# Performance work log

Measured on AMD Instinct MI355X. Metric: run time of the kernel, lower is better.

Reference implementation:

```python
import jax, jax.numpy as jnp
import numpy as np

NUM_NODES = 10000
NUM_EDGES = 640000
IN_CH = 128
HID = 128
OUT_CH = 1


def setup_inputs() -> dict:
    key = jax.random.key(0)
    ks = jax.random.split(key, 12)
    x = jax.random.normal(ks[0], (NUM_NODES, IN_CH), dtype=jnp.float32)
    edge_index = jax.random.randint(ks[1], (2, NUM_EDGES), 0, NUM_NODES, dtype=jnp.int64)
    edge_weight = jax.random.uniform(ks[2], (NUM_EDGES,), dtype=jnp.float32)
    s1 = 1.0 / np.sqrt(IN_CH)
    s2 = 1.0 / np.sqrt(HID)
    W1 = jax.random.uniform(ks[3], (HID, IN_CH), minval=-s1, maxval=s1, dtype=jnp.float32)
    b1 = jnp.zeros((HID,), dtype=jnp.float32)
    W2 = jax.random.uniform(ks[4], (HID, HID), minval=-s2, maxval=s2, dtype=jnp.float32)
    b2 = jnp.zeros((HID,), dtype=jnp.float32)
    sc = 1.0 / np.sqrt(HID * 3)
    conv_w = jax.random.uniform(ks[5], (HID, HID, 3), minval=-sc, maxval=sc, dtype=jnp.float32)
    conv_b = jax.random.uniform(ks[6], (HID,), minval=-sc, maxval=sc, dtype=jnp.float32)
    fc_w = jax.random.uniform(ks[7], (OUT_CH, HID), minval=-s2, maxval=s2, dtype=jnp.float32)
    fc_b = jax.random.uniform(ks[8], (OUT_CH,), minval=-s2, maxval=s2, dtype=jnp.float32)
    return {"x": x, "edge_index": edge_index, "edge_weight": edge_weight,
            "W1": W1, "b1": b1, "W2": W2, "b2": b2,
            "conv_w": conv_w, "conv_b": conv_b, "fc_w": fc_w, "fc_b": fc_b}


def _gcn_conv(x, row, col, norm, W, b):
    # PyG GCNConv: linear (no bias in lin), normalized scatter-add, then bias
    xw = x @ W.T                                   # [N, out]
    msg = xw[row] * norm[:, None]                  # gather + edge scale [E, out]
    out = jax.ops.segment_sum(msg, col, num_segments=NUM_NODES)
    return out + b


def reference(x, edge_index, edge_weight, W1, b1, W2, b2, conv_w, conv_b, fc_w, fc_b):
    # gcn_norm with self-loops (fill_value=1.0)
    loop = jnp.arange(NUM_NODES, dtype=edge_index.dtype)
    row = jnp.concatenate([edge_index[0], loop])
    col = jnp.concatenate([edge_index[1], loop])
    w = jnp.concatenate([edge_weight, jnp.ones((NUM_NODES,), dtype=edge_weight.dtype)])
    deg = jax.ops.segment_sum(w, col, num_segments=NUM_NODES)
    dinv = jnp.where(deg > 0, jax.lax.rsqrt(deg), 0.0)
    norm = dinv[row] * w * dinv[col]

    h = jax.nn.relu(_gcn_conv(x, row, col, norm, W1, b1))
    # dropout is identity in eval mode
    h = jax.nn.relu(_gcn_conv(h, row, col, norm, W2, b2))

    # temporal conv1d over node axis: [N,H] -> [1,H,N]
    hc = h.T[None, :, :]
    hc = jax.lax.conv_general_dilated(hc, conv_w, window_strides=(1,),
                                      padding='SAME',
                                      dimension_numbers=('NCH', 'OIH', 'NCH'))
    hc = hc + conv_b[None, :, None]
    h = hc[0].T                                    # [N, H]

    return (h @ fc_w.T + fc_b).squeeze()           # [N]
```

## Files before the change

### kernel.cpp

```cpp
#include <hip/hip_runtime.h>
#include <hip/hip_bf16.h>

#define N_NODES 10000
#define N_EDGES 640000
#define CH 128
#define NB 64
#define EPB (N_EDGES / NB)
#define NCHUNK 40
#define NPAD 10240

__global__ __launch_bounds__(256) void fused_hist_gemm(const int* __restrict__ ei,
        const float* __restrict__ x, const float* __restrict__ W1,
        int* __restrict__ hist, int* __restrict__ pcs, float* __restrict__ out,
        const float* __restrict__ conv_w, const float* __restrict__ conv_b,
        const float* __restrict__ fc_w, const float* __restrict__ fc_b,
        float* __restrict__ vbuf, float* __restrict__ c0) {
    __shared__ __align__(16) char smem[NPAD * 4];
    int t = threadIdx.x;
    int bid = blockIdx.x;
    if (bid < NB) {
        int* h = (int*)smem;
        for (int i = t; i < NPAD; i += 256) h[i] = 0;
        __syncthreads();
        int e0 = bid * EPB;
        for (int i = t; i < EPB; i += 256)
            atomicAdd(&h[ei[N_EDGES + e0 + i]], 1);
        __syncthreads();
        for (int i = t; i < N_NODES; i += 256)
            hist[bid * N_NODES + i] = h[i];
        int lane = t & 63, wave = t >> 6;
        for (int cch = wave; cch < NCHUNK; cch += 4) {
            int s = h[cch * 256 + lane] + h[cch * 256 + lane + 64]
                  + h[cch * 256 + lane + 128] + h[cch * 256 + lane + 192];
            #pragma unroll
            for (int off = 32; off > 0; off >>= 1) s += __shfl_down(s, off, 64);
            if (lane == 0) pcs[cch * NB + bid] = s;
        }
        return;
    }
    if (bid == NB + (N_NODES + 63) / 64) {
        for (int i = t; i <= 384; i += 256) {
            if (i < 384) {
                float s = 0.0f;
                for (int o = 0; o < CH; ++o) s += fc_w[o] * conv_w[o * 384 + i];
                vbuf[i] = s;
            } else {
                float s = fc_b[0];
                for (int o = 0; o < CH; ++o) s += fc_w[o] * conv_b[o];
                *c0 = s;
            }
        }
        return;
    }
    float (*As)[68]  = (float(*)[68])smem;
    float (*Ws)[132] = (float(*)[132])(smem + 32 * 68 * sizeof(float));
    int tx = t & 31;
    int ty = t >> 5;
    int row0 = (bid - NB) * 64;
    float acc[8][4] = {};
    for (int k0 = 0; k0 < 128; k0 += 32) {
        #pragma unroll
        for (int i = 0; i < 8; ++i) {
            int idx = t + i * 256;
            int r = idx >> 5, k = idx & 31;
            int gr = row0 + r;
            As[k][r] = (gr < N_NODES) ? x[gr * CH + k0 + k] : 0.0f;
        }
        #pragma unroll
        for (int i = 0; i < 16; ++i) {
            int idx = t + i * 256;
            int o = idx >> 5, k = idx & 31;
            Ws[k][o] = W1[o * CH + k0 + k];
        }
        __syncthreads();
        #pragma unroll
        for (int kk = 0; kk < 32; ++kk) {
            float a[8], w[4];
            #pragma unroll
            for (int j = 0; j < 8; ++j) a[j] = As[kk][ty * 8 + j];
            #pragma unroll
            for (int c = 0; c < 4; ++c) w[c] = Ws[kk][tx * 4 + c];
            #pragma unroll
            for (int j = 0; j < 8; ++j)
                #pragma unroll
                for (int c = 0; c < 4; ++c)
                    acc[j][c] += a[j] * w[c];
        }
        __syncthreads();
    }
    #pragma unroll
    for (int j = 0; j < 8; ++j) {
        int gr = row0 + ty * 8 + j;
        if (gr < N_NODES) {
            float4 v = make_float4(acc[j][0], acc[j][1], acc[j][2], acc[j][3]);
            *reinterpret_cast<float4*>(&out[gr * CH + tx * 4]) = v;
        }
    }
}

__global__ __launch_bounds__(256) void bofs_kernel(int* __restrict__ hist,
        const int* __restrict__ pcs, int* __restrict__ tot,
        int* __restrict__ offs) {
    __shared__ int wred[4];
    __shared__ int wsum[4];
    __shared__ int base_sh;
    int blk = blockIdx.x, t = threadIdx.x;
    int lane = t & 63, wave = t >> 6;
    int bsum = 0;
    for (int i = t; i < blk * NB; i += 256) bsum += pcs[i];
    #pragma unroll
    for (int off = 32; off > 0; off >>= 1) bsum += __shfl_down(bsum, off, 64);
    if (lane == 0) wred[wave] = bsum;
    __syncthreads();
    if (t == 0) base_sh = wred[0] + wred[1] + wred[2] + wred[3];
    int n = blk * 256 + t;
    int v = 0;
    if (n < N_NODES) {
        #pragma unroll 8
        for (int b = 0; b < NB; ++b) v += hist[b * N_NODES + n];
        tot[n] = v;
    }
    int s = v;
    #pragma unroll
    for (int off = 1; off < 64; off <<= 1) {
        int u = __shfl_up(s, off, 64);
        if (lane >= off) s += u;
    }
    if (lane == 63) wsum[wave] = s;
    __syncthreads();
    int wbase = 0;
    for (int i = 0; i < wave; ++i) wbase += wsum[i];
    if (n < N_NODES) {
        int run = base_sh + wbase + s - v;
        offs[n] = run;
        for (int b = 0; b < NB; ++b) {
            int h = hist[b * N_NODES + n];
            hist[b * N_NODES + n] = run;
            run += h;
        }
    }
}

__global__ __launch_bounds__(256) void scatter_kernel(const int* __restrict__ ei,
        const float* __restrict__ ew, const int* __restrict__ bofs,
        int2* __restrict__ erec) {
    __shared__ int cur[N_NODES];
    int b = blockIdx.x, t = threadIdx.x;
    for (int i = t; i < N_NODES; i += 256) cur[i] = bofs[b * N_NODES + i];
    __syncthreads();
    int e0 = b * EPB;
    for (int i = t; i < EPB; i += 256) {
        int e = e0 + i;
        int r = ei[e];
        int c = ei[N_EDGES + e];
        int p = atomicAdd(&cur[c], 1);
        erec[p] = make_int2(r, __float_as_int(ew[e]));
    }
}

__global__ __launch_bounds__(256) void deg_kernel(const int2* __restrict__ erec,
        const int* __restrict__ offs, const int* __restrict__ cnt,
        float* __restrict__ dinv) {
    int n = blockIdx.x * 8 + (threadIdx.x >> 5);
    int l = threadIdx.x & 31;
    int start = offs[n];
    int num = cnt[n];
    float s = 0.0f;
    for (int i = l; i < num; i += 32) s += __int_as_float(erec[start + i].y);
    #pragma unroll
    for (int off = 16; off > 0; off >>= 1) s += __shfl_down(s, off, 32);
    if (l == 0) dinv[n] = rsqrtf(s + 1.0f);
}

__global__ __launch_bounds__(256) void gemm128_kernel(const float* __restrict__ A,
                                                      const float* __restrict__ W,
                                                      float* __restrict__ out, int M) {
    __shared__ float As[32][68];
    __shared__ float Ws[32][132];
    int tid = threadIdx.x;
    int tx = tid & 31;
    int ty = tid >> 5;
    int row0 = blockIdx.x * 64;
    float acc[8][4] = {};
    for (int k0 = 0; k0 < 128; k0 += 32) {
        #pragma unroll
        for (int i = 0; i < 8; ++i) {
            int idx = tid + i * 256;
            int r = idx >> 5, k = idx & 31;
            int gr = row0 + r;
            As[k][r] = (gr < M) ? A[gr * CH + k0 + k] : 0.0f;
        }
        #pragma unroll
        for (int i = 0; i < 16; ++i) {
            int idx = tid + i * 256;
            int o = idx >> 5, k = idx & 31;
            Ws[k][o] = W[o * CH + k0 + k];
        }
        __syncthreads();
        #pragma unroll
        for (int kk = 0; kk < 32; ++kk) {
            float a[8], w[4];
            #pragma unroll
            for (int j = 0; j < 8; ++j) a[j] = As[kk][ty * 8 + j];
            #pragma unroll
            for (int c = 0; c < 4; ++c) w[c] = Ws[kk][tx * 4 + c];
            #pragma unroll
            for (int j = 0; j < 8; ++j)
                #pragma unroll
                for (int c = 0; c < 4; ++c)
                    acc[j][c] += a[j] * w[c];
        }
        __syncthreads();
    }
    #pragma unroll
    for (int j = 0; j < 8; ++j) {
        int gr = row0 + ty * 8 + j;
        if (gr < M) {
            float4 v = make_float4(acc[j][0], acc[j][1], acc[j][2], acc[j][3]);
            *reinterpret_cast<float4*>(&out[gr * CH + tx * 4]) = v;
        }
    }
}

__global__ __launch_bounds__(256) void agg_kernel(const float4* __restrict__ xw4,
        const int2* __restrict__ erec, const int* __restrict__ offs,
        const int* __restrict__ cnt, const float* __restrict__ dinv,
        const float4* __restrict__ bias4, float4* __restrict__ out4) {
    int l = threadIdx.x & 31;
    int g = threadIdx.x >> 5;
    int n = blockIdx.x * 8 + g;
    float d = dinv[n];
    float4 self = xw4[n * 32 + l];
    float4 acc = make_float4(d * self.x, d * self.y, d * self.z, d * self.w);
    int start = offs[n];
    int num = cnt[n];
    int i = 0;
    for (; i + 8 <= num; i += 8) {
        int2 r[8];
        #pragma unroll
        for (int j = 0; j < 8; ++j) r[j] = erec[start + i + j];
        float4 f[8];
        float dr[8];
        #pragma unroll
        for (int j = 0; j < 8; ++j) f[j] = xw4[r[j].x * 32 + l];
        #pragma unroll
        for (int j = 0; j < 8; ++j) dr[j] = dinv[r[j].x];
        #pragma unroll
        for (int j = 0; j < 8; ++j) {
            float v = __int_as_float(r[j].y) * dr[j];
            acc.x += v * f[j].x; acc.y += v * f[j].y;
            acc.z += v * f[j].z; acc.w += v * f[j].w;
        }
    }
    for (; i < num; ++i) {
        int2 r = erec[start + i];
        float4 f = xw4[r.x * 32 + l];
        float v = __int_as_float(r.y) * dinv[r.x];
        acc.x += v * f.x; acc.y += v * f.y; acc.z += v * f.z; acc.w += v * f.w;
    }
    float4 bb = bias4[l];
    acc.x = fmaxf(d * acc.x + bb.x, 0.0f);
    acc.y = fmaxf(d * acc.y + bb.y, 0.0f);
    acc.z = fmaxf(d * acc.z + bb.z, 0.0f);
    acc.w = fmaxf(d * acc.w + bb.w, 0.0f);
    out4[n * 32 + l] = acc;
}

__global__ __launch_bounds__(256) void convfc_kernel(const float* __restrict__ h,
        const float* __restrict__ v, const float* __restrict__ c0,
        float* __restrict__ out, int N) {
    int n = blockIdx.x * 4 + (threadIdx.x >> 6);
    int l = threadIdx.x & 63;
    if (n >= N) return;
    const float* hn = h + n * CH;
    float v0a = v[l * 3 + 0],        v1a = v[l * 3 + 1],        v2a = v[l * 3 + 2];
    float v0b = v[(l + 64) * 3 + 0], v1b = v[(l + 64) * 3 + 1], v2b = v[(l + 64) * 3 + 2];
    float p = hn[l] * v1a + hn[l + 64] * v1b;
    if (n > 0)     p += hn[l - CH] * v0a + hn[l + 64 - CH] * v0b;
    if (n < N - 1) p += hn[l + CH] * v2a + hn[l + 64 + CH] * v2b;
    #pragma unroll
    for (int off = 32; off > 0; off >>= 1) p += __shfl_down(p, off, 64);
    if (l == 0) out[n] = p + *c0;
}

extern "C" void kernel_launch(void* const* d_in, const int* in_sizes, int n_in,
                              void* d_out, int out_size, void* d_ws, size_t ws_size,
                              hipStream_t stream) {
    const float* x       = (const float*)d_in[0];
    const int*   ei      = (const int*)d_in[1];
    const float* ew      = (const float*)d_in[2];
    const float* W1      = (const float*)d_in[3];
    const float* b1      = (const float*)d_in[4];
    const float* W2      = (const float*)d_in[5];
    const float* b2      = (const float*)d_in[6];
    const float* conv_w  = (const float*)d_in[7];
    const float* conv_b  = (const float*)d_in[8];
    const float* fc_w    = (const float*)d_in[9];
    const float* fc_b    = (const float*)d_in[10];
    float* out = (float*)d_out;

    float* bufA   = (float*)d_ws;
    float* bufB   = bufA + N_NODES * CH;
    int2*  erec   = (int2*)(bufB + N_NODES * CH);
    int*   hist   = (int*)(erec + N_EDGES);
    int*   pcs    = hist + NB * N_NODES;
    int*   tot    = pcs + NCHUNK * NB;
    int*   offs   = tot + N_NODES;
    float* dinv   = (float*)(offs + N_NODES);
    float* vbuf   = dinv + N_NODES;
    float* c0     = vbuf + 384;

    const int gemm_grid = (N_NODES + 63) / 64;

    fused_hist_gemm<<<NB + gemm_grid + 1, 256, 0, stream>>>(ei, x, W1, hist, pcs,
            bufA, conv_w, conv_b, fc_w, fc_b, vbuf, c0);
    bofs_kernel<<<NCHUNK, 256, 0, stream>>>(hist, pcs, tot, offs);
    scatter_kernel<<<NB, 256, 0, stream>>>(ei, ew, hist, erec);
    deg_kernel<<<N_NODES / 8, 256, 0, stream>>>(erec, offs, tot, dinv);

    agg_kernel<<<N_NODES / 8, 256, 0, stream>>>((const float4*)bufA, erec, offs, tot,
                                                dinv, (const float4*)b1, (float4*)bufB);
    gemm128_kernel<<<gemm_grid, 256, 0, stream>>>(bufB, W2, bufA, N_NODES);
    agg_kernel<<<N_NODES / 8, 256, 0, stream>>>((const float4*)bufA, erec, offs, tot,
                                                dinv, (const float4*)b2, (float4*)bufB);
    convfc_kernel<<<(N_NODES + 3) / 4, 256, 0, stream>>>(bufB, vbuf, c0, out, N_NODES);
}
```

Measured before the change: 219.5 us.

## Fold degree into histogram pass, prenormalize edges, fuse aggregation with W2 GEMM

The histogram pass now also accumulates weighted degrees in shared memory, so the prefix kernel can compute dinv directly and the separate degree kernel is removed. The scatter kernel stores the fully normalized edge weight dinv[r]*w*dinv[c], which removes the per-edge dinv gather from both aggregation passes. The first aggregation is fused with the second layer's linear transform: each block multiplies its 8 aggregated rows by W2 straight from shared memory, removing a kernel launch and a round trip of the hidden matrix. The cost is doubled LDS use in the histogram blocks, an extra float histogram written and read, and W2 being read from global memory by every block without tiling.

```diff
diff --git a/kernel.cpp b/kernel.cpp
--- a/kernel.cpp
+++ b/kernel.cpp
@@ -10,24 +10,33 @@
 #define NPAD 10240
 
 __global__ __launch_bounds__(256) void fused_hist_gemm(const int* __restrict__ ei,
+        const float* __restrict__ ew,
         const float* __restrict__ x, const float* __restrict__ W1,
-        int* __restrict__ hist, int* __restrict__ pcs, float* __restrict__ out,
+        int* __restrict__ hist, float* __restrict__ dhist, int* __restrict__ pcs,
+        float* __restrict__ out,
         const float* __restrict__ conv_w, const float* __restrict__ conv_b,
         const float* __restrict__ fc_w, const float* __restrict__ fc_b,
         float* __restrict__ vbuf, float* __restrict__ c0) {
-    __shared__ __align__(16) char smem[NPAD * 4];
+    __shared__ __align__(16) char smem[NPAD * 8];
     int t = threadIdx.x;
     int bid = blockIdx.x;
     if (bid < NB) {
         int* h = (int*)smem;
-        for (int i = t; i < NPAD; i += 256) h[i] = 0;
+        float* hf = (float*)(smem + NPAD * 4);
+        for (int i = t; i < 2 * NPAD; i += 256) ((int*)smem)[i] = 0;
         __syncthreads();
         int e0 = bid * EPB;
-        for (int i = t; i < EPB; i += 256)
-            atomicAdd(&h[ei[N_EDGES + e0 + i]], 1);
+        for (int i = t; i < EPB; i += 256) {
+            int e = e0 + i;
+            int c = ei[N_EDGES + e];
+            atomicAdd(&h[c], 1);
+            atomicAdd(&hf[c], ew[e]);
+        }
         __syncthreads();
-        for (int i = t; i < N_NODES; i += 256)
+        for (int i = t; i < N_NODES; i += 256) {
             hist[bid * N_NODES + i] = h[i];
+            dhist[bid * N_NODES + i] = hf[i];
+        }
         int lane = t & 63, wave = t >> 6;
         for (int cch = wave; cch < NCHUNK; cch += 4) {
             int s = h[cch * 256 + lane] + h[cch * 256 + lane + 64]
@@ -99,8 +108,8 @@
 }
 
 __global__ __launch_bounds__(256) void bofs_kernel(int* __restrict__ hist,
-        const int* __restrict__ pcs, int* __restrict__ tot,
-        int* __restrict__ offs) {
+        const float* __restrict__ dhist, const int* __restrict__ pcs,
+        int* __restrict__ tot, int* __restrict__ offs, float* __restrict__ dinv) {
     __shared__ int wred[4];
     __shared__ int wsum[4];
     __shared__ int base_sh;
@@ -116,9 +125,14 @@
     int n = blk * 256 + t;
     int v = 0;
     if (n < N_NODES) {
+        float dsum = 0.0f;
         #pragma unroll 8
-        for (int b = 0; b < NB; ++b) v += hist[b * N_NODES + n];
+        for (int b = 0; b < NB; ++b) {
+            v += hist[b * N_NODES + n];
+            dsum += dhist[b * N_NODES + n];
+        }
         tot[n] = v;
+        dinv[n] = rsqrtf(dsum + 1.0f);
     }
     int s = v;
     #pragma unroll
@@ -142,84 +156,92 @@
 }
 
 __global__ __launch_bounds__(256) void scatter_kernel(const int* __restrict__ ei,
-        const float* __restrict__ ew, const int* __restrict__ bofs,
-        int2* __restrict__ erec) {
+        const float* __restrict__ ew, const float* __restrict__ dinv,
+        const int* __restrict__ bofs, int2* __restrict__ erec) {
     __shared__ int cur[N_NODES];
+    __shared__ float di[N_NODES];
     int b = blockIdx.x, t = threadIdx.x;
-    for (int i = t; i < N_NODES; i += 256) cur[i] = bofs[b * N_NODES + i];
+    for (int i = t; i < N_NODES; i += 256) {
+        cur[i] = bofs[b * N_NODES + i];
+        di[i] = dinv[i];
+    }
     __syncthreads();
     int e0 = b * EPB;
     for (int i = t; i < EPB; i += 256) {
         int e = e0 + i;
         int r = ei[e];
         int c = ei[N_EDGES + e];
+        float v = di[r] * ew[e] * di[c];
         int p = atomicAdd(&cur[c], 1);
-        erec[p] = make_int2(r, __float_as_int(ew[e]));
-    }
-}
-
-__global__ __launch_bounds__(256) void deg_kernel(const int2* __restrict__ erec,
-        const int* __restrict__ offs, const int* __restrict__ cnt,
-        float* __restrict__ dinv) {
-    int n = blockIdx.x * 8 + (threadIdx.x >> 5);
+        erec[p] = make_int2(r, __float_as_int(v));
+    }
+}
+
+__global__ __launch_bounds__(256) void agg_gemm_kernel(const float4* __restrict__ xw4,
+        const int2* __restrict__ erec, const int* __restrict__ offs,
+        const int* __restrict__ cnt, const float* __restrict__ dinv,
+        const float4* __restrict__ bias4, const float* __restrict__ W2,
+        float* __restrict__ out) {
+    __shared__ float hs[8][128];
     int l = threadIdx.x & 31;
+    int g = threadIdx.x >> 5;
+    int n = blockIdx.x * 8 + g;
+    float d = dinv[n];
+    float dd = d * d;
+    float4 self = xw4[n * 32 + l];
+    float4 acc = make_float4(dd * self.x, dd * self.y, dd * self.z, dd * self.w);
     int start = offs[n];
     int num = cnt[n];
-    float s = 0.0f;
-    for (int i = l; i < num; i += 32) s += __int_as_float(erec[start + i].y);
-    #pragma unroll
-    for (int off = 16; off > 0; off >>= 1) s += __shfl_down(s, off, 32);
-    if (l == 0) dinv[n] = rsqrtf(s + 1.0f);
-}
-
-__global__ __launch_bounds__(256) void gemm128_kernel(const float* __restrict__ A,
-                                                      const float* __restrict__ W,
-                                                      float* __restrict__ out, int M) {
-    __shared__ float As[32][68];
-    __shared__ float Ws[32][132];
-    int tid = threadIdx.x;
-    int tx = tid & 31;
-    int ty = tid >> 5;
-    int row0 = blockIdx.x * 64;
-    float acc[8][4] = {};
-    for (int k0 = 0; k0 < 128; k0 += 32) {
-        #pragma unroll
-        for (int i = 0; i < 8; ++i) {
-            int idx = tid + i * 256;
-            int r = idx >> 5, k = idx & 31;
-            int gr = row0 + r;
-            As[k][r] = (gr < M) ? A[gr * CH + k0 + k] : 0.0f;
-        }
-        #pragma unroll
-        for (int i = 0; i < 16; ++i) {
-            int idx = tid + i * 256;
-            int o = idx >> 5, k = idx & 31;
-            Ws[k][o] = W[o * CH + k0 + k];
-        }
-        __syncthreads();
-        #pragma unroll
-        for (int kk = 0; kk < 32; ++kk) {
-            float a[8], w[4];
-            #pragma unroll
-            for (int j = 0; j < 8; ++j) a[j] = As[kk][ty * 8 + j];
-            #pragma unroll
-            for (int c = 0; c < 4; ++c) w[c] = Ws[kk][tx * 4 + c];
-            #pragma unroll
-            for (int j = 0; j < 8; ++j)
-                #pragma unroll
-                for (int c = 0; c < 4; ++c)
-                    acc[j][c] += a[j] * w[c];
-        }
-        __syncthreads();
-    }
-    #pragma unroll
-    for (int j = 0; j < 8; ++j) {
-        int gr = row0 + ty * 8 + j;
-        if (gr < M) {
-            float4 v = make_float4(acc[j][0], acc[j][1], acc[j][2], acc[j][3]);
-            *reinterpret_cast<float4*>(&out[gr * CH + tx * 4]) = v;
-        }
-    }
+    int i = 0;
+    for (; i + 8 <= num; i += 8) {
+        int2 r[8];
+        #pragma unroll
+        for (int j = 0; j < 8; ++j) r[j] = erec[start + i + j];
+        float4 f[8];
+        #pragma unroll
+        for (int j = 0; j < 8; ++j) f[j] = xw4[r[j].x * 32 + l];
+        #pragma unroll
+        for (int j = 0; j < 8; ++j) {
+            float v = __int_as_float(r[j].y);
+            acc.x += v * f[j].x; acc.y += v * f[j].y;
+            acc.z += v * f[j].z; acc.w += v * f[j].w;
+        }
+    }
+    for (; i < num; ++i) {
+        int2 r = erec[start + i];
+        float4 f = xw4[r.x * 32 + l];
+        float v = __int_as_float(r.y);
+        acc.x += v * f.x; acc.y += v * f.y; acc.z += v * f.z; acc.w += v * f.w;
+    }
+    float4 bb = bias4[l];
+    acc.x = fmaxf(acc.x + bb.x, 0.0f);
+    acc.y = fmaxf(acc.y + bb.y, 0.0f);
+    acc.z = fmaxf(acc.z + bb.z, 0.0f);
+    acc.w = fmaxf(acc.w + bb.w, 0.0f);
+    *reinterpret_cast<float4*>(&hs[g][4 * l]) = acc;
+    __syncthreads();
+    int o = threadIdx.x & 127;
+    int rg = threadIdx.x >> 7;
+    const float4* w4p = reinterpret_cast<const float4*>(&W2[o * CH]);
+    const float4* h0p = reinterpret_cast<const float4*>(&hs[rg * 4 + 0][0]);
+    const float4* h1p = reinterpret_cast<const float4*>(&hs[rg * 4 + 1][0]);
+    const float4* h2p = reinterpret_cast<const float4*>(&hs[rg * 4 + 2][0]);
+    const float4* h3p = reinterpret_cast<const float4*>(&hs[rg * 4 + 3][0]);
+    float a0 = 0.0f, a1 = 0.0f, a2 = 0.0f, a3 = 0.0f;
+    #pragma unroll 8
+    for (int k4 = 0; k4 < 32; ++k4) {
+        float4 w = w4p[k4];
+        float4 h0 = h0p[k4], h1 = h1p[k4], h2 = h2p[k4], h3 = h3p[k4];
+        a0 += w.x * h0.x + w.y * h0.y + w.z * h0.z + w.w * h0.w;
+        a1 += w.x * h1.x + w.y * h1.y + w.z * h1.z + w.w * h1.w;
+        a2 += w.x * h2.x + w.y * h2.y + w.z * h2.z + w.w * h2.w;
+        a3 += w.x * h3.x + w.y * h3.y + w.z * h3.z + w.w * h3.w;
+    }
+    int nb = blockIdx.x * 8 + rg * 4;
+    out[(nb + 0) * CH + o] = a0;
+    out[(nb + 1) * CH + o] = a1;
+    out[(nb + 2) * CH + o] = a2;
+    out[(nb + 3) * CH + o] = a3;
 }
 
 __global__ __launch_bounds__(256) void agg_kernel(const float4* __restrict__ xw4,
@@ -230,8 +252,9 @@
     int g = threadIdx.x >> 5;
     int n = blockIdx.x * 8 + g;
     float d = dinv[n];
+    float dd = d * d;
     float4 self = xw4[n * 32 + l];
-    float4 acc = make_float4(d * self.x, d * self.y, d * self.z, d * self.w);
+    float4 acc = make_float4(dd * self.x, dd * self.y, dd * self.z, dd * self.w);
     int start = offs[n];
     int num = cnt[n];
     int i = 0;
@@ -240,14 +263,11 @@
         #pragma unroll
         for (int j = 0; j < 8; ++j) r[j] = erec[start + i + j];
         float4 f[8];
-        float dr[8];
         #pragma unroll
         for (int j = 0; j < 8; ++j) f[j] = xw4[r[j].x * 32 + l];
         #pragma unroll
-        for (int j = 0; j < 8; ++j) dr[j] = dinv[r[j].x];
-        #pragma unroll
         for (int j = 0; j < 8; ++j) {
-            float v = __int_as_float(r[j].y) * dr[j];
+            float v = __int_as_float(r[j].y);
             acc.x += v * f[j].x; acc.y += v * f[j].y;
             acc.z += v * f[j].z; acc.w += v * f[j].w;
         }
@@ -255,14 +275,14 @@
     for (; i < num; ++i) {
         int2 r = erec[start + i];
         float4 f = xw4[r.x * 32 + l];
-        float v = __int_as_float(r.y) * dinv[r.x];
+        float v = __int_as_float(r.y);
         acc.x += v * f.x; acc.y += v * f.y; acc.z += v * f.z; acc.w += v * f.w;
     }
     float4 bb = bias4[l];
-    acc.x = fmaxf(d * acc.x + bb.x, 0.0f);
-    acc.y = fmaxf(d * acc.y + bb.y, 0.0f);
-    acc.z = fmaxf(d * acc.z + bb.z, 0.0f);
-    acc.w = fmaxf(d * acc.w + bb.w, 0.0f);
+    acc.x = fmaxf(acc.x + bb.x, 0.0f);
+    acc.y = fmaxf(acc.y + bb.y, 0.0f);
+    acc.z = fmaxf(acc.z + bb.z, 0.0f);
+    acc.w = fmaxf(acc.w + bb.w, 0.0f);
     out4[n * 32 + l] = acc;
 }
 
@@ -303,7 +323,8 @@
     float* bufB   = bufA + N_NODES * CH;
     int2*  erec   = (int2*)(bufB + N_NODES * CH);
     int*   hist   = (int*)(erec + N_EDGES);
-    int*   pcs    = hist + NB * N_NODES;
+    float* dhist  = (float*)(hist + NB * N_NODES);
+    int*   pcs    = (int*)(dhist + NB * N_NODES);
     int*   tot    = pcs + NCHUNK * NB;
     int*   offs   = tot + N_NODES;
     float* dinv   = (float*)(offs + N_NODES);
@@ -312,16 +333,13 @@
 
     const int gemm_grid = (N_NODES + 63) / 64;
 
-    fused_hist_gemm<<<NB + gemm_grid + 1, 256, 0, stream>>>(ei, x, W1, hist, pcs,
-            bufA, conv_w, conv_b, fc_w, fc_b, vbuf, c0);
-    bofs_kernel<<<NCHUNK, 256, 0, stream>>>(hist, pcs, tot, offs);
-    scatter_kernel<<<NB, 256, 0, stream>>>(ei, ew, hist, erec);
-    deg_kernel<<<N_NODES / 8, 256, 0, stream>>>(erec, offs, tot, dinv);
-
-    agg_kernel<<<N_NODES / 8, 256, 0, stream>>>((const float4*)bufA, erec, offs, tot,
-                                                dinv, (const float4*)b1, (float4*)bufB);
-    gemm128_kernel<<<gemm_grid, 256, 0, stream>>>(bufB, W2, bufA, N_NODES);
-    agg_kernel<<<N_NODES / 8, 256, 0, stream>>>((const float4*)bufA, erec, offs, tot,
-                                                dinv, (const float4*)b2, (float4*)bufB);
-    convfc_kernel<<<(N_NODES + 3) / 4, 256, 0, stream>>>(bufB, vbuf, c0, out, N_NODES);
-}
+    fused_hist_gemm<<<NB + gemm_grid + 1, 256, 0, stream>>>(ei, ew, x, W1,
+            hist, dhist, pcs, bufA, conv_w, conv_b, fc_w, fc_b, vbuf, c0);
+    bofs_kernel<<<NCHUNK, 256, 0, stream>>>(hist, dhist, pcs, tot, offs, dinv);
+    scatter_kernel<<<NB, 256, 0, stream>>>(ei, ew, dinv, hist, erec);
+    agg_gemm_kernel<<<N_NODES / 8, 256, 0, stream>>>((const float4*)bufA, erec, offs,
+            tot, dinv, (const float4*)b1, W2, bufB);
+    agg_kernel<<<N_NODES / 8, 256, 0, stream>>>((const float4*)bufB, erec, offs, tot,
+                                                dinv, (const float4*)b2, (float4*)bufA);
+    convfc_kernel<<<(N_NODES + 3) / 4, 256, 0, stream>>>(bufA, vbuf, c0, out, N_NODES);
+}
```

After: 207.3 us. 1.06x faster.
